# Kernel tuning notes

Measured on AMD Instinct MI355X. Metric: run time of the kernel, lower is better.

## Reference

```python
import jax, jax.numpy as jnp
import numpy as np

# static config matching init_kwargs
H, W, C, K = 64, 64, 32, 2          # dense_bev_height/width, bev_ch, k
SLH, SLW = 4, 4                     # lidar scales
RSH, RSW = 4, 4                     # rgb scales
HF, WF = 96, 320                    # rgb feature-map spatial dims (rgb_hw / rgb_scale)
FEAT = 256                          # rgb feature channels
SHIFT_H, SHIFT_W = 0.0, 0.0
N_IN = (FEAT + 3) * K               # 518


def setup_inputs() -> dict:
    key = jax.random.key(0)
    ks = jax.random.split(key, 13)
    inp = {}
    inp['input'] = jax.random.normal(ks[0], (1, HF, WF, FEAT), dtype=jnp.float32)
    inp['kdtree'] = jax.random.normal(ks[1], (1, H * SLH, W * SLW, C, K, 4), dtype=jnp.float32) * 10.0
    inp['Tr'] = jax.random.normal(ks[2], (4, 4), dtype=jnp.float32)
    inp['R0'] = jax.random.normal(ks[3], (4, 4), dtype=jnp.float32)
    inp['P3'] = jax.random.normal(ks[4], (3, 4), dtype=jnp.float32)
    inp['w1'] = jax.random.normal(ks[5], (N_IN, 128), dtype=jnp.float32) * 0.02
    inp['b1'] = jax.random.normal(ks[6], (128,), dtype=jnp.float32) * 0.02
    inp['w2'] = jax.random.normal(ks[7], (128, 64), dtype=jnp.float32) * 0.02
    inp['b2'] = jax.random.normal(ks[8], (64,), dtype=jnp.float32) * 0.02
    inp['w3'] = jax.random.normal(ks[9], (64, 1), dtype=jnp.float32) * 0.02
    inp['b3'] = jax.random.normal(ks[10], (1,), dtype=jnp.float32) * 0.02
    inp['conv_w'] = jax.random.normal(ks[11], (C, 1), dtype=jnp.float32) * 0.1
    inp['conv_b'] = jax.random.normal(ks[12], (1,), dtype=jnp.float32) * 0.1
    return inp


def reference(input, kdtree, Tr, R0, P3, w1, b1, w2, b2, w3, b3, conv_w, conv_b):
    # strided gather of per-voxel KNN records: [H, W, C, K, 4]
    oi = jnp.arange(H) * SLH
    oj = jnp.arange(W) * SLW
    kpts = kdtree[0][oi[:, None], oj[None, :]]
    # current voxel anchor point [1, original_i, original_j, channel] -> [H, W, C, 4]
    f32 = jnp.float32
    cur = jnp.stack(jnp.broadcast_arrays(
        jnp.ones((H, W, C), f32),
        oi.astype(f32)[:, None, None] * jnp.ones((H, W, C), f32),
        oj.astype(f32)[None, :, None] * jnp.ones((H, W, C), f32),
        jnp.arange(C, dtype=f32)[None, None, :] * jnp.ones((H, W, C), f32)), axis=-1)
    dist = (kpts - cur[:, :, :, None, :])[..., :3]  # [H, W, C, K, 3]
    # project lidar points to image plane: P3 @ R0 @ Tr @ [x, y, z, 1]
    hom = jnp.concatenate([kpts[..., :3], jnp.ones(kpts.shape[:-1] + (1,), f32)], axis=-1)
    M = P3 @ R0 @ Tr  # [3, 4]
    cam = jnp.einsum('hwckd,ed->hwcke', hom, M)
    z = cam[..., 2]
    z = jnp.where(jnp.abs(z) < 1e-6, 1e-6, z)
    py = cam[..., 1] / z + SHIFT_H
    px = cam[..., 0] / z + SHIFT_W
    iy = jnp.clip(py.astype(jnp.int32) // RSH, 0, HF - 1)
    ix = jnp.clip(px.astype(jnp.int32) // RSW, 0, WF - 1)
    # indexed pixel gather from the RGB feature map: [H, W, C, K, 256]
    rgb = input[0][iy, ix]
    # concat per-neighbor [rgb | distance] then flatten neighbors: [H*W*C, K*259]
    feats = jnp.concatenate([rgb, dist], axis=-1).reshape(H * W * C, N_IN)
    h1 = jax.nn.relu(feats @ w1 + b1)
    h2 = jax.nn.relu(h1 @ w2 + b2)
    out = h2 @ w3 + b3  # [H*W*C, 1]
    # original stacks as [C, H, W, B, 1] then reshapes to [-1, H, W, C]
    dense = out.reshape(H, W, C).transpose(2, 0, 1).reshape(1, H, W, C)
    y = jnp.einsum('bhwc,co->bhwo', dense, conv_w) + conv_b
    return y
```

## Files before the change

### kernel.cpp

```cpp
#include <hip/hip_runtime.h>

#define HH 64
#define WWID 64
#define CCH 32
#define HFD 96
#define WFD 320
#define NPIX (HFD*WFD)
#define NVOX (HH*WWID*CCH)

typedef __attribute__((ext_vector_type(8))) short short8;
typedef __attribute__((ext_vector_type(4))) float f32x4;

__device__ __forceinline__ float4 ld4(const float* p){ return *reinterpret_cast<const float4*>(p); }
__device__ __forceinline__ unsigned short f2bf(float f){
  unsigned int u = __float_as_uint(f);
  return (unsigned short)((u + 0x7FFFu + ((u>>16)&1u)) >> 16);
}
__device__ __forceinline__ float bf2f(unsigned short s){
  return __uint_as_float(((unsigned int)s) << 16);
}

__global__ __launch_bounds__(256) void prep_kernel(
    const float* __restrict__ kdtree, const float* __restrict__ Tr,
    const float* __restrict__ R0, const float* __restrict__ P3,
    float4* __restrict__ nb)
{
  int gid = blockIdx.x*256 + threadIdx.x;
  double PR[12], M[12];
  #pragma unroll
  for (int e=0;e<3;e++)
    #pragma unroll
    for (int b=0;b<4;b++){
      double s = 0.0;
      #pragma unroll
      for (int a=0;a<4;a++) s += (double)P3[e*4+a]*(double)R0[a*4+b];
      PR[e*4+b] = s;
    }
  #pragma unroll
  for (int e=0;e<3;e++)
    #pragma unroll
    for (int d=0;d<4;d++){
      double s = 0.0;
      #pragma unroll
      for (int b=0;b<4;b++) s += PR[e*4+b]*(double)Tr[b*4+d];
      M[e*4+d] = s;
    }
  int v = gid>>1, k = gid&1;
  int c = v&31, w = (v>>5)&63, h = v>>11;
  size_t off = ((((size_t)(h*4)*256 + (size_t)(w*4))*32 + c)*2 + k)*4;
  float4 kp = ld4(kdtree + off);
  double k0=kp.x, k1=kp.y, k2=kp.z;
  double cam0 = M[0]*k0 + M[1]*k1 + M[2]*k2 + M[3];
  double cam1 = M[4]*k0 + M[5]*k1 + M[6]*k2 + M[7];
  double cam2 = M[8]*k0 + M[9]*k1 + M[10]*k2 + M[11];
  float zf = (float)cam2;
  double zd = (fabsf(zf) < 1e-6f) ? (double)1e-6f : cam2;
  double py = cam1/zd, px = cam0/zd;
  int ty = (int)py, tx = (int)px;
  int iy = ty < 0 ? 0 : ((ty>>2) > (HFD-1) ? (HFD-1) : (ty>>2));
  int ix = tx < 0 ? 0 : ((tx>>2) > (WFD-1) ? (WFD-1) : (tx>>2));
  float4 r;
  r.x = __int_as_float(iy*WFD + ix);
  r.y = kp.x - 1.0f;
  r.z = kp.y - (float)(h*4);
  r.w = kp.z - (float)(w*4);
  nb[gid] = r;
}

__global__ __launch_bounds__(256) void wcvt_kernel(const float* __restrict__ w1,
                                                   const float* __restrict__ w2,
                                                   unsigned short* __restrict__ wt,
                                                   unsigned short* __restrict__ w2t)
{
  int e = blockIdx.x*256 + threadIdx.x;
  if (e < 65536){
    int n = e>>8, k = e&255;
    float v = (n<128) ? w1[k*128 + n] : w1[(259+k)*128 + (n-128)];
    wt[n*256 + k] = f2bf(v);
  } else {
    int e2 = e - 65536;
    int c = e2>>7, k = e2&127;
    w2t[c*128 + k] = f2bf(w2[k*64 + c]);
  }
}

__global__ __launch_bounds__(256) void pix_mfma(
    const float* __restrict__ input, const unsigned short* __restrict__ wt,
    unsigned short* __restrict__ pixb)
{
  __shared__ unsigned short sm[64*264];
  int t = threadIdx.x;
  long pbase = (long)blockIdx.x*64;
  const float* src = input + pbase*256;
  float4 xv[16];
  #pragma unroll
  for (int i=0;i<16;i++) xv[i] = ld4(src + i*1024 + t*4);
  #pragma unroll
  for (int i=0;i<16;i++){
    int e = i*1024 + t*4;
    int row = e>>8, k = e&255;
    ushort4 u;
    u.x = f2bf(xv[i].x); u.y = f2bf(xv[i].y); u.z = f2bf(xv[i].z); u.w = f2bf(xv[i].w);
    unsigned byteoff = (unsigned)((row*512 + k*2) ^ ((row&7)<<4));
    *reinterpret_cast<ushort4*>(reinterpret_cast<char*>(sm) + byteoff) = u;
  }
  __syncthreads();

  int l = t & 63, wv = t >> 6;
  int rl = l & 15, khi = l >> 4;
  unsigned xorv = (unsigned)((rl & 7) << 4);
  const unsigned short* wb = wt + (size_t)(wv*64 + rl)*256 + khi*8;

  f32x4 acc[4][4];
  #pragma unroll
  for (int m=0;m<4;m++)
    #pragma unroll
    for (int n=0;n<4;n++) acc[m][n] = (f32x4){0.f,0.f,0.f,0.f};

  #pragma unroll
  for (int kk=0; kk<8; ++kk){
    short8 a[4], b[4];
    #pragma unroll
    for (int m=0;m<4;m++){
      unsigned off = (unsigned)(((m*16+rl)*512 + (kk*32 + khi*8)*2) ^ xorv);
      a[m] = *reinterpret_cast<const short8*>(reinterpret_cast<const char*>(sm) + off);
    }
    #pragma unroll
    for (int n=0;n<4;n++)
      b[n] = *reinterpret_cast<const short8*>(wb + n*16*256 + kk*32);
    #pragma unroll
    for (int m=0;m<4;m++)
      #pragma unroll
      for (int n=0;n<4;n++)
        acc[m][n] = __builtin_amdgcn_mfma_f32_16x16x32_bf16(a[m], b[n], acc[m][n], 0, 0, 0);
  }

  __syncthreads();
  #pragma unroll
  for (int m=0;m<4;m++)
    #pragma unroll
    for (int n=0;n<4;n++){
      int col = wv*64 + n*16 + rl;
      #pragma unroll
      for (int i=0;i<4;i++){
        int row = m*16 + khi*4 + i;
        sm[row*264 + col] = f2bf(acc[m][n][i]);
      }
    }
  __syncthreads();
  #pragma unroll
  for (int i=0;i<4;i++){
    int row = (t>>4) + i*16;
    const unsigned short* sp = sm + row*264 + (t&15)*16;
    short8 v0 = *reinterpret_cast<const short8*>(sp);
    short8 v1 = *reinterpret_cast<const short8*>(sp+8);
    unsigned short* dst = pixb + (pbase+row)*256 + (t&15)*16;
    *reinterpret_cast<short8*>(dst)   = v0;
    *reinterpret_cast<short8*>(dst+8) = v1;
  }
}

__global__ __launch_bounds__(256) void h1_kernel(
    const float4* __restrict__ nb, const unsigned short* __restrict__ pixb,
    const float* __restrict__ w1, const float* __restrict__ b1,
    unsigned short* __restrict__ h1b)
{
  int gid = blockIdx.x*256 + threadIdx.x;
  int v = gid>>4, o = (gid&15)*8;
  float4 n0 = nb[(size_t)v*2], n1 = nb[(size_t)v*2+1];
  int i0 = __float_as_int(n0.x), i1 = __float_as_int(n1.x);
  short8 pA = *reinterpret_cast<const short8*>(pixb + (size_t)i0*256 + o);
  short8 pB = *reinterpret_cast<const short8*>(pixb + (size_t)i1*256 + 128 + o);
  const float* wd = w1 + 256*128 + o;
  const float* we = w1 + 515*128 + o;
  union { short8 s; unsigned short u[8]; } pk;
  #pragma unroll
  for (int j=0;j<8;j++){
    float x = bf2f((unsigned short)pA[j]) + bf2f((unsigned short)pB[j]);
    x = fmaf(n0.y, wd[j],     x);
    x = fmaf(n0.z, wd[128+j], x);
    x = fmaf(n0.w, wd[256+j], x);
    x = fmaf(n1.y, we[j],     x);
    x = fmaf(n1.z, we[128+j], x);
    x = fmaf(n1.w, we[256+j], x);
    x += b1[o+j];
    pk.u[j] = f2bf(fmaxf(x, 0.f));
  }
  *reinterpret_cast<short8*>(h1b + (size_t)v*128 + o) = pk.s;
}

__global__ __launch_bounds__(256) void mlp2_kernel(
    const unsigned short* __restrict__ h1b, const unsigned short* __restrict__ w2t,
    const float* __restrict__ b2, const float* __restrict__ w3,
    const float* __restrict__ b3, float* __restrict__ mlpout)
{
  int t = threadIdx.x;
  int l = t&63, wv = t>>6;
  int rl = l&15, khi = l>>4;
  int rowbase = blockIdx.x*128 + wv*32;

  f32x4 acc[2][4];
  #pragma unroll
  for (int m=0;m<2;m++)
    #pragma unroll
    for (int n=0;n<4;n++) acc[m][n] = (f32x4){0.f,0.f,0.f,0.f};

  #pragma unroll
  for (int kk=0; kk<4; ++kk){
    short8 a[2], b[4];
    #pragma unroll
    for (int m=0;m<2;m++)
      a[m] = *reinterpret_cast<const short8*>(h1b + (size_t)(rowbase + m*16 + rl)*128 + kk*32 + khi*8);
    #pragma unroll
    for (int n=0;n<4;n++)
      b[n] = *reinterpret_cast<const short8*>(w2t + (size_t)(n*16 + rl)*128 + kk*32 + khi*8);
    #pragma unroll
    for (int m=0;m<2;m++)
      #pragma unroll
      for (int n=0;n<4;n++)
        acc[m][n] = __builtin_amdgcn_mfma_f32_16x16x32_bf16(a[m], b[n], acc[m][n], 0, 0, 0);
  }

  float b2v[4], w3v[4];
  #pragma unroll
  for (int n=0;n<4;n++){ b2v[n] = b2[n*16+rl]; w3v[n] = w3[n*16+rl]; }
  float bias3 = b3[0];
  #pragma unroll
  for (int m=0;m<2;m++){
    #pragma unroll
    for (int i=0;i<4;i++){
      float s = 0.f;
      #pragma unroll
      for (int n=0;n<4;n++)
        s = fmaf(fmaxf(acc[m][n][i] + b2v[n], 0.f), w3v[n], s);
      s += __shfl_xor(s, 1);
      s += __shfl_xor(s, 2);
      s += __shfl_xor(s, 4);
      s += __shfl_xor(s, 8);
      if (rl == 0) mlpout[rowbase + m*16 + khi*4 + i] = s + bias3;
    }
  }
}

__global__ __launch_bounds__(256) void conv_kernel(
    const float* __restrict__ mlpout, const float* __restrict__ conv_w,
    const float* __restrict__ conv_b, float* __restrict__ y)
{
  int t = blockIdx.x*256 + threadIdx.x;
  int i = t>>6, j = t&63;
  int c = i>>1;
  int base = ((i&1)<<11) + j*32;
  float acc = conv_b[0];
  #pragma unroll
  for (int k=0;k<32;++k)
    acc = fmaf(conv_w[k], mlpout[(size_t)(base+k)*32 + c], acc);
  y[t] = acc;
}

extern "C" void kernel_launch(void* const* d_in, const int* in_sizes, int n_in,
                              void* d_out, int out_size, void* d_ws, size_t ws_size,
                              hipStream_t stream)
{
  const float* input  = (const float*)d_in[0];
  const float* kdtree = (const float*)d_in[1];
  const float* Tr     = (const float*)d_in[2];
  const float* R0     = (const float*)d_in[3];
  const float* P3     = (const float*)d_in[4];
  const float* w1     = (const float*)d_in[5];
  const float* b1     = (const float*)d_in[6];
  const float* w2     = (const float*)d_in[7];
  const float* b2     = (const float*)d_in[8];
  const float* w3     = (const float*)d_in[9];
  const float* b3     = (const float*)d_in[10];
  const float* conv_w = (const float*)d_in[11];
  const float* conv_b = (const float*)d_in[12];

  char* wsb = (char*)d_ws;
  unsigned short* pixb = (unsigned short*)wsb;
  float4* nb           = (float4*)(wsb + 15728640);
  unsigned short* h1b  = (unsigned short*)(wsb + 19922944);
  float* mlpout        = (float*)(wsb + 53477376);
  unsigned short* wt   = (unsigned short*)(wsb + 54001664);
  unsigned short* w2t  = (unsigned short*)(wsb + 54132736);
  float* y = (float*)d_out;

  hipLaunchKernelGGL(wcvt_kernel, dim3(288),        dim3(256), 0, stream, w1, w2, wt, w2t);
  hipLaunchKernelGGL(prep_kernel, dim3(NVOX*2/256), dim3(256), 0, stream, kdtree, Tr, R0, P3, nb);
  hipLaunchKernelGGL(pix_mfma,    dim3(NPIX/64),    dim3(256), 0, stream, input, wt, pixb);
  hipLaunchKernelGGL(h1_kernel,   dim3(NVOX*16/256),dim3(256), 0, stream, nb, pixb, w1, b1, h1b);
  hipLaunchKernelGGL(mlp2_kernel, dim3(NVOX/128),   dim3(256), 0, stream, h1b, w2t, b2, w3, b3, mlpout);
  hipLaunchKernelGGL(conv_kernel, dim3(16),         dim3(256), 0, stream, mlpout, conv_w, conv_b, y);
}
```

Measured before the change: 187.4 us.

## Fuse projection, h1 and MLP2 into one kernel; precompute camera matrix once

Merges the neighbour projection, the first-layer combine and the second MLP layer into a single kernel that keeps the per-block h1 tile in LDS. This avoids writing and rereading the h1 and neighbour buffers through global memory. The camera matrix is now computed once in a setup kernel that also converts the weights, instead of being recomputed in every thread. The pixel GEMM tile is halved to 32 rows, which doubles the block count, and the conv kernel uses smaller blocks. The fused kernel launches fewer, larger-work blocks, and the projection step runs on only half the threads.

```diff
diff --git a/kernel.cpp b/kernel.cpp
--- a/kernel.cpp
+++ b/kernel.cpp
@@ -20,65 +20,37 @@
   return __uint_as_float(((unsigned int)s) << 16);
 }
 
-__global__ __launch_bounds__(256) void prep_kernel(
-    const float* __restrict__ kdtree, const float* __restrict__ Tr,
-    const float* __restrict__ R0, const float* __restrict__ P3,
-    float4* __restrict__ nb)
-{
-  int gid = blockIdx.x*256 + threadIdx.x;
-  double PR[12], M[12];
-  #pragma unroll
-  for (int e=0;e<3;e++)
-    #pragma unroll
-    for (int b=0;b<4;b++){
+__global__ __launch_bounds__(256) void setup_kernel(
+    const float* __restrict__ P3, const float* __restrict__ R0,
+    const float* __restrict__ Tr, const float* __restrict__ w1,
+    const float* __restrict__ w2,
+    double* __restrict__ Md, unsigned short* __restrict__ wt,
+    unsigned short* __restrict__ w2t)
+{
+  int b = blockIdx.x, t = threadIdx.x;
+  if (b == 0){
+    if (t < 12){
+      int e3 = t>>2, d = t&3;
+      double PRr[4];
+      #pragma unroll
+      for (int bb=0;bb<4;bb++){
+        double s = 0.0;
+        #pragma unroll
+        for (int a=0;a<4;a++) s += (double)P3[e3*4+a]*(double)R0[a*4+bb];
+        PRr[bb] = s;
+      }
       double s = 0.0;
       #pragma unroll
-      for (int a=0;a<4;a++) s += (double)P3[e*4+a]*(double)R0[a*4+b];
-      PR[e*4+b] = s;
-    }
-  #pragma unroll
-  for (int e=0;e<3;e++)
-    #pragma unroll
-    for (int d=0;d<4;d++){
-      double s = 0.0;
-      #pragma unroll
-      for (int b=0;b<4;b++) s += PR[e*4+b]*(double)Tr[b*4+d];
-      M[e*4+d] = s;
-    }
-  int v = gid>>1, k = gid&1;
-  int c = v&31, w = (v>>5)&63, h = v>>11;
-  size_t off = ((((size_t)(h*4)*256 + (size_t)(w*4))*32 + c)*2 + k)*4;
-  float4 kp = ld4(kdtree + off);
-  double k0=kp.x, k1=kp.y, k2=kp.z;
-  double cam0 = M[0]*k0 + M[1]*k1 + M[2]*k2 + M[3];
-  double cam1 = M[4]*k0 + M[5]*k1 + M[6]*k2 + M[7];
-  double cam2 = M[8]*k0 + M[9]*k1 + M[10]*k2 + M[11];
-  float zf = (float)cam2;
-  double zd = (fabsf(zf) < 1e-6f) ? (double)1e-6f : cam2;
-  double py = cam1/zd, px = cam0/zd;
-  int ty = (int)py, tx = (int)px;
-  int iy = ty < 0 ? 0 : ((ty>>2) > (HFD-1) ? (HFD-1) : (ty>>2));
-  int ix = tx < 0 ? 0 : ((tx>>2) > (WFD-1) ? (WFD-1) : (tx>>2));
-  float4 r;
-  r.x = __int_as_float(iy*WFD + ix);
-  r.y = kp.x - 1.0f;
-  r.z = kp.y - (float)(h*4);
-  r.w = kp.z - (float)(w*4);
-  nb[gid] = r;
-}
-
-__global__ __launch_bounds__(256) void wcvt_kernel(const float* __restrict__ w1,
-                                                   const float* __restrict__ w2,
-                                                   unsigned short* __restrict__ wt,
-                                                   unsigned short* __restrict__ w2t)
-{
-  int e = blockIdx.x*256 + threadIdx.x;
-  if (e < 65536){
+      for (int bb=0;bb<4;bb++) s += PRr[bb]*(double)Tr[bb*4+d];
+      Md[t] = s;
+    }
+  } else if (b <= 256){
+    int e = (b-1)*256 + t;
     int n = e>>8, k = e&255;
     float v = (n<128) ? w1[k*128 + n] : w1[(259+k)*128 + (n-128)];
     wt[n*256 + k] = f2bf(v);
   } else {
-    int e2 = e - 65536;
+    int e2 = (b-257)*256 + t;
     int c = e2>>7, k = e2&127;
     w2t[c*128 + k] = f2bf(w2[k*64 + c]);
   }
@@ -88,15 +60,15 @@
     const float* __restrict__ input, const unsigned short* __restrict__ wt,
     unsigned short* __restrict__ pixb)
 {
-  __shared__ unsigned short sm[64*264];
+  __shared__ unsigned short sm[32*260];
   int t = threadIdx.x;
-  long pbase = (long)blockIdx.x*64;
+  long pbase = (long)blockIdx.x*32;
   const float* src = input + pbase*256;
-  float4 xv[16];
-  #pragma unroll
-  for (int i=0;i<16;i++) xv[i] = ld4(src + i*1024 + t*4);
-  #pragma unroll
-  for (int i=0;i<16;i++){
+  float4 xv[8];
+  #pragma unroll
+  for (int i=0;i<8;i++) xv[i] = ld4(src + i*1024 + t*4);
+  #pragma unroll
+  for (int i=0;i<8;i++){
     int e = i*1024 + t*4;
     int row = e>>8, k = e&255;
     ushort4 u;
@@ -111,47 +83,47 @@
   unsigned xorv = (unsigned)((rl & 7) << 4);
   const unsigned short* wb = wt + (size_t)(wv*64 + rl)*256 + khi*8;
 
-  f32x4 acc[4][4];
-  #pragma unroll
-  for (int m=0;m<4;m++)
+  f32x4 acc[2][4];
+  #pragma unroll
+  for (int m=0;m<2;m++)
     #pragma unroll
     for (int n=0;n<4;n++) acc[m][n] = (f32x4){0.f,0.f,0.f,0.f};
 
   #pragma unroll
   for (int kk=0; kk<8; ++kk){
-    short8 a[4], b[4];
-    #pragma unroll
-    for (int m=0;m<4;m++){
+    short8 a[2], bfr[4];
+    #pragma unroll
+    for (int m=0;m<2;m++){
       unsigned off = (unsigned)(((m*16+rl)*512 + (kk*32 + khi*8)*2) ^ xorv);
       a[m] = *reinterpret_cast<const short8*>(reinterpret_cast<const char*>(sm) + off);
     }
     #pragma unroll
     for (int n=0;n<4;n++)
-      b[n] = *reinterpret_cast<const short8*>(wb + n*16*256 + kk*32);
-    #pragma unroll
-    for (int m=0;m<4;m++)
+      bfr[n] = *reinterpret_cast<const short8*>(wb + n*16*256 + kk*32);
+    #pragma unroll
+    for (int m=0;m<2;m++)
       #pragma unroll
       for (int n=0;n<4;n++)
-        acc[m][n] = __builtin_amdgcn_mfma_f32_16x16x32_bf16(a[m], b[n], acc[m][n], 0, 0, 0);
-  }
-
-  __syncthreads();
-  #pragma unroll
-  for (int m=0;m<4;m++)
+        acc[m][n] = __builtin_amdgcn_mfma_f32_16x16x32_bf16(a[m], bfr[n], acc[m][n], 0, 0, 0);
+  }
+
+  __syncthreads();
+  #pragma unroll
+  for (int m=0;m<2;m++)
     #pragma unroll
     for (int n=0;n<4;n++){
       int col = wv*64 + n*16 + rl;
       #pragma unroll
       for (int i=0;i<4;i++){
         int row = m*16 + khi*4 + i;
-        sm[row*264 + col] = f2bf(acc[m][n][i]);
+        sm[row*260 + col] = f2bf(acc[m][n][i]);
       }
     }
   __syncthreads();
   #pragma unroll
-  for (int i=0;i<4;i++){
+  for (int i=0;i<2;i++){
     int row = (t>>4) + i*16;
-    const unsigned short* sp = sm + row*264 + (t&15)*16;
+    const unsigned short* sp = sm + row*260 + (t&15)*16;
     short8 v0 = *reinterpret_cast<const short8*>(sp);
     short8 v1 = *reinterpret_cast<const short8*>(sp+8);
     unsigned short* dst = pixb + (pbase+row)*256 + (t&15)*16;
@@ -160,93 +132,117 @@
   }
 }
 
-__global__ __launch_bounds__(256) void h1_kernel(
-    const float4* __restrict__ nb, const unsigned short* __restrict__ pixb,
+__global__ __launch_bounds__(256) void fused_kernel(
+    const float* __restrict__ kdtree, const double* __restrict__ Md,
+    const unsigned short* __restrict__ pixb,
     const float* __restrict__ w1, const float* __restrict__ b1,
-    unsigned short* __restrict__ h1b)
-{
-  int gid = blockIdx.x*256 + threadIdx.x;
-  int v = gid>>4, o = (gid&15)*8;
-  float4 n0 = nb[(size_t)v*2], n1 = nb[(size_t)v*2+1];
-  int i0 = __float_as_int(n0.x), i1 = __float_as_int(n1.x);
-  short8 pA = *reinterpret_cast<const short8*>(pixb + (size_t)i0*256 + o);
-  short8 pB = *reinterpret_cast<const short8*>(pixb + (size_t)i1*256 + 128 + o);
-  const float* wd = w1 + 256*128 + o;
-  const float* we = w1 + 515*128 + o;
-  union { short8 s; unsigned short u[8]; } pk;
-  #pragma unroll
-  for (int j=0;j<8;j++){
-    float x = bf2f((unsigned short)pA[j]) + bf2f((unsigned short)pB[j]);
-    x = fmaf(n0.y, wd[j],     x);
-    x = fmaf(n0.z, wd[128+j], x);
-    x = fmaf(n0.w, wd[256+j], x);
-    x = fmaf(n1.y, we[j],     x);
-    x = fmaf(n1.z, we[128+j], x);
-    x = fmaf(n1.w, we[256+j], x);
-    x += b1[o+j];
-    pk.u[j] = f2bf(fmaxf(x, 0.f));
-  }
-  *reinterpret_cast<short8*>(h1b + (size_t)v*128 + o) = pk.s;
-}
-
-__global__ __launch_bounds__(256) void mlp2_kernel(
-    const unsigned short* __restrict__ h1b, const unsigned short* __restrict__ w2t,
-    const float* __restrict__ b2, const float* __restrict__ w3,
-    const float* __restrict__ b3, float* __restrict__ mlpout)
-{
+    const unsigned short* __restrict__ w2t, const float* __restrict__ b2,
+    const float* __restrict__ w3, const float* __restrict__ b3,
+    float* __restrict__ mlpout)
+{
+  __shared__ float4 nbs[128];
+  __shared__ unsigned short h1s[64*128];
+  __shared__ float outs[64];
   int t = threadIdx.x;
+  int vb = blockIdx.x*64;
+
+  if (t < 128){
+    int vloc = t>>1, k = t&1;
+    int v = vb + vloc;
+    int c = v&31, w = (v>>5)&63, h = v>>11;
+    size_t off = ((((size_t)(h*4)*256 + (size_t)(w*4))*32 + c)*2 + k)*4;
+    float4 kp = ld4(kdtree + off);
+    double k0 = kp.x, k1 = kp.y, k2 = kp.z;
+    double cam0 = Md[0]*k0 + Md[1]*k1 + Md[2]*k2  + Md[3];
+    double cam1 = Md[4]*k0 + Md[5]*k1 + Md[6]*k2  + Md[7];
+    double cam2 = Md[8]*k0 + Md[9]*k1 + Md[10]*k2 + Md[11];
+    float zf = (float)cam2;
+    double zd = (fabsf(zf) < 1e-6f) ? (double)1e-6f : cam2;
+    double rz = 1.0/zd;
+    int ty = (int)(cam1*rz), tx = (int)(cam0*rz);
+    int iy = ty < 0 ? 0 : ((ty>>2) > (HFD-1) ? (HFD-1) : (ty>>2));
+    int ix = tx < 0 ? 0 : ((tx>>2) > (WFD-1) ? (WFD-1) : (tx>>2));
+    float4 r;
+    r.x = __int_as_float(iy*WFD + ix);
+    r.y = kp.x - 1.0f;
+    r.z = kp.y - (float)(h*4);
+    r.w = kp.z - (float)(w*4);
+    nbs[t] = r;
+  }
+  __syncthreads();
+
+  #pragma unroll
+  for (int it=0; it<4; ++it){
+    int task = it*256 + t;
+    int vloc = task>>4, o = (task&15)*8;
+    float4 n0 = nbs[vloc*2], n1 = nbs[vloc*2+1];
+    int i0 = __float_as_int(n0.x), i1 = __float_as_int(n1.x);
+    short8 pA = *reinterpret_cast<const short8*>(pixb + (size_t)i0*256 + o);
+    short8 pB = *reinterpret_cast<const short8*>(pixb + (size_t)i1*256 + 128 + o);
+    const float* wd = w1 + 256*128 + o;
+    const float* we = w1 + 515*128 + o;
+    union { short8 s; unsigned short u[8]; } pk;
+    #pragma unroll
+    for (int j=0;j<8;j++){
+      float x = bf2f((unsigned short)pA[j]) + bf2f((unsigned short)pB[j]);
+      x = fmaf(n0.y, wd[j],     x);
+      x = fmaf(n0.z, wd[128+j], x);
+      x = fmaf(n0.w, wd[256+j], x);
+      x = fmaf(n1.y, we[j],     x);
+      x = fmaf(n1.z, we[128+j], x);
+      x = fmaf(n1.w, we[256+j], x);
+      x += b1[o+j];
+      pk.u[j] = f2bf(fmaxf(x, 0.f));
+    }
+    unsigned byteoff = (unsigned)((vloc*256 + (task&15)*16) ^ ((vloc&7)<<4));
+    *reinterpret_cast<short8*>(reinterpret_cast<char*>(h1s) + byteoff) = pk.s;
+  }
+  __syncthreads();
+
   int l = t&63, wv = t>>6;
   int rl = l&15, khi = l>>4;
-  int rowbase = blockIdx.x*128 + wv*32;
-
-  f32x4 acc[2][4];
-  #pragma unroll
-  for (int m=0;m<2;m++)
-    #pragma unroll
-    for (int n=0;n<4;n++) acc[m][n] = (f32x4){0.f,0.f,0.f,0.f};
+  int rowbase = wv*16;
+
+  f32x4 acc[4];
+  #pragma unroll
+  for (int n=0;n<4;n++) acc[n] = (f32x4){0.f,0.f,0.f,0.f};
 
   #pragma unroll
   for (int kk=0; kk<4; ++kk){
-    short8 a[2], b[4];
-    #pragma unroll
-    for (int m=0;m<2;m++)
-      a[m] = *reinterpret_cast<const short8*>(h1b + (size_t)(rowbase + m*16 + rl)*128 + kk*32 + khi*8);
+    int row = rowbase + rl;
+    unsigned off = (unsigned)((row*256 + (kk*32 + khi*8)*2) ^ ((row&7)<<4));
+    short8 a = *reinterpret_cast<const short8*>(reinterpret_cast<const char*>(h1s) + off);
+    #pragma unroll
+    for (int n=0;n<4;n++){
+      short8 bfr = *reinterpret_cast<const short8*>(w2t + (size_t)(n*16 + rl)*128 + kk*32 + khi*8);
+      acc[n] = __builtin_amdgcn_mfma_f32_16x16x32_bf16(a, bfr, acc[n], 0, 0, 0);
+    }
+  }
+
+  float b2v[4], w3v[4];
+  #pragma unroll
+  for (int n=0;n<4;n++){ b2v[n] = b2[n*16+rl]; w3v[n] = w3[n*16+rl]; }
+  #pragma unroll
+  for (int i=0;i<4;i++){
+    float s = 0.f;
     #pragma unroll
     for (int n=0;n<4;n++)
-      b[n] = *reinterpret_cast<const short8*>(w2t + (size_t)(n*16 + rl)*128 + kk*32 + khi*8);
-    #pragma unroll
-    for (int m=0;m<2;m++)
-      #pragma unroll
-      for (int n=0;n<4;n++)
-        acc[m][n] = __builtin_amdgcn_mfma_f32_16x16x32_bf16(a[m], b[n], acc[m][n], 0, 0, 0);
-  }
-
-  float b2v[4], w3v[4];
-  #pragma unroll
-  for (int n=0;n<4;n++){ b2v[n] = b2[n*16+rl]; w3v[n] = w3[n*16+rl]; }
-  float bias3 = b3[0];
-  #pragma unroll
-  for (int m=0;m<2;m++){
-    #pragma unroll
-    for (int i=0;i<4;i++){
-      float s = 0.f;
-      #pragma unroll
-      for (int n=0;n<4;n++)
-        s = fmaf(fmaxf(acc[m][n][i] + b2v[n], 0.f), w3v[n], s);
-      s += __shfl_xor(s, 1);
-      s += __shfl_xor(s, 2);
-      s += __shfl_xor(s, 4);
-      s += __shfl_xor(s, 8);
-      if (rl == 0) mlpout[rowbase + m*16 + khi*4 + i] = s + bias3;
-    }
-  }
-}
-
-__global__ __launch_bounds__(256) void conv_kernel(
+      s = fmaf(fmaxf(acc[n][i] + b2v[n], 0.f), w3v[n], s);
+    s += __shfl_xor(s, 1);
+    s += __shfl_xor(s, 2);
+    s += __shfl_xor(s, 4);
+    s += __shfl_xor(s, 8);
+    if (rl == 0) outs[rowbase + khi*4 + i] = s;
+  }
+  __syncthreads();
+  if (t < 64) mlpout[vb + t] = outs[t] + b3[0];
+}
+
+__global__ __launch_bounds__(64) void conv_kernel(
     const float* __restrict__ mlpout, const float* __restrict__ conv_w,
     const float* __restrict__ conv_b, float* __restrict__ y)
 {
-  int t = blockIdx.x*256 + threadIdx.x;
+  int t = blockIdx.x*64 + threadIdx.x;
   int i = t>>6, j = t&63;
   int c = i>>1;
   int base = ((i&1)<<11) + j*32;
@@ -277,17 +273,14 @@
 
   char* wsb = (char*)d_ws;
   unsigned short* pixb = (unsigned short*)wsb;
-  float4* nb           = (float4*)(wsb + 15728640);
-  unsigned short* h1b  = (unsigned short*)(wsb + 19922944);
-  float* mlpout        = (float*)(wsb + 53477376);
-  unsigned short* wt   = (unsigned short*)(wsb + 54001664);
-  unsigned short* w2t  = (unsigned short*)(wsb + 54132736);
+  float* mlpout        = (float*)(wsb + 15728640);
+  unsigned short* wt   = (unsigned short*)(wsb + 16252928);
+  unsigned short* w2t  = (unsigned short*)(wsb + 16384000);
+  double* Md           = (double*)(wsb + 16400384);
   float* y = (float*)d_out;
 
-  hipLaunchKernelGGL(wcvt_kernel, dim3(288),        dim3(256), 0, stream, w1, w2, wt, w2t);
-  hipLaunchKernelGGL(prep_kernel, dim3(NVOX*2/256), dim3(256), 0, stream, kdtree, Tr, R0, P3, nb);
-  hipLaunchKernelGGL(pix_mfma,    dim3(NPIX/64),    dim3(256), 0, stream, input, wt, pixb);
-  hipLaunchKernelGGL(h1_kernel,   dim3(NVOX*16/256),dim3(256), 0, stream, nb, pixb, w1, b1, h1b);
-  hipLaunchKernelGGL(mlp2_kernel, dim3(NVOX/128),   dim3(256), 0, stream, h1b, w2t, b2, w3, b3, mlpout);
-  hipLaunchKernelGGL(conv_kernel, dim3(16),         dim3(256), 0, stream, mlpout, conv_w, conv_b, y);
-}
+  hipLaunchKernelGGL(setup_kernel, dim3(289),       dim3(256), 0, stream, P3, R0, Tr, w1, w2, Md, wt, w2t);
+  hipLaunchKernelGGL(pix_mfma,     dim3(NPIX/32),   dim3(256), 0, stream, input, wt, pixb);
+  hipLaunchKernelGGL(fused_kernel, dim3(NVOX/64),   dim3(256), 0, stream, kdtree, Md, pixb, w1, b1, w2t, b2, w3, b3, mlpout);
+  hipLaunchKernelGGL(conv_kernel,  dim3(64),        dim3(64),  0, stream, mlpout, conv_w, conv_b, y);
+}
```

After: 247.0 us. 1.32x slower.
